# Performance work log

Measured on AMD Instinct MI355X. Metric: run time of the kernel, lower is better.

The kernel has to match this reference:

```python
import jax, jax.numpy as jnp
import numpy as np

B, M, IN_DIM = 8, 2048, 512
N_HEAD, ATTN_DIM = 8, 64
HEAD_DIM = N_HEAD * ATTN_DIM  # 512
SCALE = HEAD_DIM ** (-0.5)


def setup_inputs() -> dict:
    key = jax.random.key(0)
    ks = jax.random.split(key, 5)
    s = IN_DIM ** -0.5
    return {
        "x": jax.random.normal(ks[0], (B, M, IN_DIM), dtype=jnp.float32),
        "Wq": jax.random.normal(ks[1], (IN_DIM, HEAD_DIM), dtype=jnp.float32) * s,
        "Wk": jax.random.normal(ks[2], (IN_DIM, HEAD_DIM), dtype=jnp.float32) * s,
        "Wv": jax.random.normal(ks[3], (IN_DIM, HEAD_DIM), dtype=jnp.float32) * s,
        "Wo": jax.random.normal(ks[4], (HEAD_DIM, IN_DIM), dtype=jnp.float32) * s,
        "bo": jnp.zeros((IN_DIM,), dtype=jnp.float32),
    }


def _split_heads(t):
    # [B, M, H*D] -> [B, H, M, D]
    b, m, _ = t.shape
    return t.reshape(b, m, N_HEAD, ATTN_DIM).transpose(0, 2, 1, 3)


def reference(x, Wq, Wk, Wv, Wo, bo):
    q = _split_heads(x @ Wq)  # bhmd
    k = _split_heads(x @ Wk)
    v = _split_heads(x @ Wv)
    # Faithful to source: logits DIVIDED by scale=head_dim**-0.5 (i.e. * sqrt(head_dim))
    logits = jnp.einsum('bhid,bhjd->bhij', q, k) / SCALE
    scores = jax.nn.softmax(logits, axis=-1)
    weighted = jnp.einsum('bhij,bhjd->bhid', scores, v)  # [B,H,M,D]
    merged = weighted.transpose(0, 2, 1, 3).reshape(x.shape[0], x.shape[1], HEAD_DIM)
    return merged @ Wo + bo
```

## Files before the change

### kernel.cpp

```cpp
#include <hip/hip_runtime.h>
#include <hip/hip_bf16.h>
#include <cstdint>

#define DI __device__ __forceinline__

typedef __attribute__((ext_vector_type(8))) short bf16x8;
typedef __attribute__((ext_vector_type(4))) short s16x4;
typedef __attribute__((ext_vector_type(4))) float f32x4;
typedef __attribute__((ext_vector_type(2))) int   i32x2;

static constexpr int BATCH = 8, SEQ = 2048;
static constexpr int ROWS = BATCH * SEQ;
static constexpr float SCALE_Q = (float)(22.627416997969522 * 1.4426950408889634);

DI short f2bf(float f) { __hip_bfloat16 h = __float2bfloat16(f); return *reinterpret_cast<short*>(&h); }
DI float bf2f(short s) { __hip_bfloat16 h; *reinterpret_cast<short*>(&h) = s; return __bfloat162float(h); }
DI unsigned pack2(float a, float b) {
  return (unsigned)(unsigned short)f2bf(a) | ((unsigned)(unsigned short)f2bf(b) << 16);
}

DI void gload_lds16(const void* gp, void* lp) {
  __builtin_amdgcn_global_load_lds(
      (__attribute__((address_space(1))) void*)const_cast<void*>(gp),
      (__attribute__((address_space(3))) void*)lp, 16, 0, 0);
}
DI f32x4 mfma16(bf16x8 a, bf16x8 b, f32x4 c) {
  return __builtin_amdgcn_mfma_f32_16x16x32_bf16(a, b, c, 0, 0, 0);
}

__global__ __launch_bounds__(256)
void prep_x(const float* __restrict__ x, short* __restrict__ xh, short* __restrict__ xl)
{
  const int g0 = blockIdx.x * 1024 + threadIdx.x;
#pragma unroll
  for (int i = 0; i < 4; ++i) {
    int g = g0 + i * 256;
    const float4 v = *reinterpret_cast<const float4*>(x + (size_t)g * 4);
    s16x4 h4, l4;
#pragma unroll
    for (int j = 0; j < 4; ++j) {
      float f = ((const float*)&v)[j];
      short hb = f2bf(f);
      h4[j] = hb;
      l4[j] = f2bf(f - bf2f(hb));
    }
    *reinterpret_cast<s16x4*>(xh + (size_t)g * 4) = h4;
    *reinterpret_cast<s16x4*>(xl + (size_t)g * 4) = l4;
  }
}

__global__ __launch_bounds__(256)
void prep_w(const float* __restrict__ Wq, const float* __restrict__ Wk,
            const float* __restrict__ Wv, const float* __restrict__ Wo,
            short* __restrict__ Wqk_hi, short* __restrict__ Wqk_lo,
            short* __restrict__ Wv_t, short* __restrict__ Wo_t)
{
  __shared__ float t[64][65];
  const int blk = blockIdx.x;
  const int mat = blk >> 6;
  const int tile = blk & 63;
  const int tn = (tile & 7) * 64;
  const int tk = (tile >> 3) * 64;
  const float* src = mat == 0 ? Wq : mat == 1 ? Wk : mat == 2 ? Wv : Wo;
  const float scale = (mat == 0) ? SCALE_Q : 1.0f;
  const int tid = threadIdx.x;
#pragma unroll
  for (int i = 0; i < 16; ++i) {
    int idx = i * 256 + tid;
    t[idx >> 6][idx & 63] = src[(size_t)(tk + (idx >> 6)) * 512 + tn + (idx & 63)];
  }
  __syncthreads();
#pragma unroll
  for (int i = 0; i < 16; ++i) {
    int idx = i * 256 + tid;
    int nn = idx >> 6, kk = idx & 63;
    float v = t[kk][nn] * scale;
    short hb = f2bf(v);
    size_t o = (size_t)(tn + nn) * 512 + (tk + kk);
    if (mat <= 1) {
      Wqk_hi[(size_t)mat * 512 * 512 + o] = hb;
      Wqk_lo[(size_t)mat * 512 * 512 + o] = f2bf(v - bf2f(hb));
    } else if (mat == 2) Wv_t[o] = hb;
    else Wo_t[o] = hb;
  }
}

template<int MODE>
__global__ __launch_bounds__(256, 2)
void gemm_kern(const short* __restrict__ Axh, const short* __restrict__ Axl,
               const short* __restrict__ Bhg, const short* __restrict__ Blg,
               short* __restrict__ O0h, short* __restrict__ O0l,
               short* __restrict__ O1h, short* __restrict__ O1l,
               float* __restrict__ Of, const float* __restrict__ bias)
{
  constexpr bool SPLIT = (MODE == 0);
  __shared__ __align__(16) short Ah[128 * 32];
  __shared__ __align__(16) short Bh[128 * 32];
  __shared__ __align__(16) short Al[SPLIT ? 128 * 32 : 16];
  __shared__ __align__(16) short Bl[SPLIT ? 128 * 32 : 16];

  const int tid = threadIdx.x;
  const int wave = tid >> 6, lane = tid & 63, lo = lane & 15, hi4 = lane >> 4;
  const int wr = wave >> 1, wc = wave & 1;
  const int m0 = blockIdx.y * 128, n0 = blockIdx.x * 128;

  f32x4 acc[4][4] = {};

  for (int kt = 0; kt < 16; ++kt) {
    __syncthreads();
#pragma unroll
    for (int is = 0; is < 2; ++is) {
      int rowl = is * 64 + wave * 16 + (lane >> 2);
      int chunk = (lane & 3) ^ ((rowl >> 1) & 3);
      size_t ab = ((size_t)(m0 + rowl) * 512 + kt * 32) * 2 + chunk * 16;
      gload_lds16((const char*)Axh + ab, (char*)Ah + is * 4096 + wave * 1024);
      if constexpr (SPLIT)
        gload_lds16((const char*)Axl + ab, (char*)Al + is * 4096 + wave * 1024);
      size_t gb = ((size_t)(n0 + rowl) * 512 + kt * 32) * 2 + chunk * 16;
      gload_lds16((const char*)Bhg + gb, (char*)Bh + is * 4096 + wave * 1024);
      if constexpr (SPLIT)
        gload_lds16((const char*)Blg + gb, (char*)Bl + is * 4096 + wave * 1024);
    }
    __syncthreads();
    bf16x8 a_h[4], a_l[4], b_h[4], b_l[4];
#pragma unroll
    for (int m = 0; m < 4; ++m) {
      int ar = wr * 64 + m * 16 + lo;
      int off = ar * 64 + ((hi4 ^ ((ar >> 1) & 3)) << 4);
      a_h[m] = *reinterpret_cast<const bf16x8*>((const char*)Ah + off);
      if constexpr (SPLIT) a_l[m] = *reinterpret_cast<const bf16x8*>((const char*)Al + off);
    }
#pragma unroll
    for (int n = 0; n < 4; ++n) {
      int br = wc * 64 + n * 16 + lo;
      int off = br * 64 + ((hi4 ^ ((br >> 1) & 3)) << 4);
      b_h[n] = *reinterpret_cast<const bf16x8*>((const char*)Bh + off);
      if constexpr (SPLIT) b_l[n] = *reinterpret_cast<const bf16x8*>((const char*)Bl + off);
    }
    __builtin_amdgcn_s_setprio(1);
#pragma unroll
    for (int m = 0; m < 4; ++m)
#pragma unroll
      for (int n = 0; n < 4; ++n) {
        acc[m][n] = mfma16(a_h[m], b_h[n], acc[m][n]);
        if constexpr (SPLIT) {
          acc[m][n] = mfma16(a_h[m], b_l[n], acc[m][n]);
          acc[m][n] = mfma16(a_l[m], b_h[n], acc[m][n]);
        }
      }
    __builtin_amdgcn_s_setprio(0);
  }
#pragma unroll
  for (int m = 0; m < 4; ++m)
#pragma unroll
    for (int n = 0; n < 4; ++n) {
      if constexpr (MODE == 1) {
        int cg = n0 + wc * 64 + n * 16 + lo;
        int rgb = m0 + wr * 64 + m * 16 + hi4 * 4;
        int bh = (rgb >> 11) * 8 + (cg >> 6);
        s16x4 vt4;
#pragma unroll
        for (int j = 0; j < 4; ++j) vt4[j] = f2bf(acc[m][n][j]);
        size_t o = ((size_t)(bh * 64 + (cg & 63))) * 2048 + (rgb & 2047);
        *reinterpret_cast<s16x4*>(O0h + o) = vt4;
      } else {
#pragma unroll
        for (int j = 0; j < 4; ++j) {
          int rg = m0 + wr * 64 + m * 16 + hi4 * 4 + j;
          int cg = n0 + wc * 64 + n * 16 + lo;
          float v = acc[m][n][j];
          if constexpr (MODE == 2) {
            Of[(size_t)rg * 512 + cg] = v + bias[cg];
          } else {
            int mat = cg >> 9;
            int c9 = cg & 511;
            size_t o = ((size_t)((rg >> 11) * 8 + (c9 >> 6)) * 2048 + (rg & 2047)) * 64 + (c9 & 63);
            short hb = f2bf(v);
            short lb = f2bf(v - bf2f(hb));
            if (mat == 0) { O0h[o] = hb; O0l[o] = lb; }
            else          { O1h[o] = hb; O1l[o] = lb; }
          }
        }
      }
    }
}

__global__ __launch_bounds__(256, 2)
void attn_kern(const short* __restrict__ Qh, const short* __restrict__ Ql,
               const short* __restrict__ Kh, const short* __restrict__ Kl,
               const short* __restrict__ VTg, short* __restrict__ Og)
{
  __shared__ __align__(16) short Ksh[2][64 * 64];
  __shared__ __align__(16) short Ksl[2][64 * 64];
  __shared__ __align__(16) short Vts[2][64 * 64];
  __shared__ __align__(16) short Ps[4][1024];

  const int bh = blockIdx.y, qt = blockIdx.x;
  const int tid = threadIdx.x, wave = tid >> 6, lane = tid & 63, lo = lane & 15, hi4 = lane >> 4;
  const int q0 = qt * 64;

  const size_t qoff = ((size_t)bh * 2048 + q0 + wave * 16 + lo) * 64;
  bf16x8 qh[2], ql[2];
#pragma unroll
  for (int kk = 0; kk < 2; ++kk) {
    qh[kk] = *reinterpret_cast<const bf16x8*>(Qh + qoff + kk * 32 + hi4 * 8);
    ql[kk] = *reinterpret_cast<const bf16x8*>(Ql + qoff + kk * 32 + hi4 * 8);
  }

  f32x4 acc_o[4] = {};
  float m_run = -3.0e38f, l_run = 0.f;

  short* pw = &Ps[wave][0];

  auto STAGE = [&](int kt, int buf) {
#pragma unroll
    for (int is = 0; is < 2; ++is) {
      int rowl = is * 32 + wave * 8 + (lane >> 3);
      int chunk = (lane & 7) ^ (rowl & 7);
      size_t gbK = ((size_t)bh * 2048 + kt * 64 + rowl) * 128 + chunk * 16;
      gload_lds16((const char*)Kh + gbK, (char*)&Ksh[buf][0] + is * 4096 + wave * 1024);
      gload_lds16((const char*)Kl + gbK, (char*)&Ksl[buf][0] + is * 4096 + wave * 1024);
      size_t gbV = (((size_t)bh * 64 + rowl) * 2048 + kt * 64) * 2 + chunk * 16;
      gload_lds16((const char*)VTg + gbV, (char*)&Vts[buf][0] + is * 4096 + wave * 1024);
    }
  };

  STAGE(0, 0);
  __syncthreads();

  for (int kt = 0; kt < 32; ++kt) {
    const int cur = kt & 1;
    if (kt < 31) STAGE(kt + 1, cur ^ 1);

    f32x4 s[4];
    __builtin_amdgcn_s_setprio(1);
#pragma unroll
    for (int kb = 0; kb < 4; ++kb) {
      f32x4 t = {0.f, 0.f, 0.f, 0.f};
#pragma unroll
      for (int kk = 0; kk < 2; ++kk) {
        int krow = kb * 16 + lo;
        int off = krow * 128 + ((kk * 64 + hi4 * 16) ^ ((krow & 7) << 4));
        bf16x8 kh8 = *reinterpret_cast<const bf16x8*>((const char*)&Ksh[cur][0] + off);
        bf16x8 kl8 = *reinterpret_cast<const bf16x8*>((const char*)&Ksl[cur][0] + off);
        t = mfma16(kh8, qh[kk], t);
        t = mfma16(kl8, qh[kk], t);
        t = mfma16(kh8, ql[kk], t);
      }
      s[kb] = t;
    }
    __builtin_amdgcn_s_setprio(0);

    float mt = s[0][0];
#pragma unroll
    for (int kb = 0; kb < 4; ++kb)
#pragma unroll
      for (int j = 0; j < 4; ++j) mt = fmaxf(mt, s[kb][j]);
    mt = fmaxf(mt, __shfl_xor(mt, 16));
    mt = fmaxf(mt, __shfl_xor(mt, 32));
    if (!__all(mt - m_run <= 8.0f)) {
      float mn = fmaxf(m_run, mt);
      float corr = exp2f(m_run - mn);
      m_run = mn;
      l_run *= corr;
#pragma unroll
      for (int j = 0; j < 4; ++j) {
        float cj = __shfl(corr, hi4 * 4 + j);
#pragma unroll
        for (int db = 0; db < 4; ++db) acc_o[db][j] *= cj;
      }
    }
    float ls = 0.f;
#pragma unroll
    for (int kb = 0; kb < 4; ++kb)
#pragma unroll
      for (int j = 0; j < 4; ++j) {
        float p = exp2f(s[kb][j] - m_run);
        s[kb][j] = p;
        ls += p;
      }
    ls += __shfl_xor(ls, 16);
    ls += __shfl_xor(ls, 32);
    l_run += ls;

#pragma unroll
    for (int kb = 0; kb < 4; ++kb) {
      i32x2 w;
      w.x = (int)pack2(s[kb][0], s[kb][1]);
      w.y = (int)pack2(s[kb][2], s[kb][3]);
      int off = lo * 128 + ((kb * 32 + hi4 * 8) ^ ((lo & 7) << 4));
      *reinterpret_cast<i32x2*>((char*)pw + off) = w;
    }
    __builtin_amdgcn_sched_barrier(0);
    bf16x8 pa[2];
#pragma unroll
    for (int kk = 0; kk < 2; ++kk) {
      int off = lo * 128 + ((kk * 64 + hi4 * 16) ^ ((lo & 7) << 4));
      pa[kk] = *reinterpret_cast<const bf16x8*>((const char*)pw + off);
    }

    __builtin_amdgcn_s_setprio(1);
#pragma unroll
    for (int db = 0; db < 4; ++db) {
#pragma unroll
      for (int kk = 0; kk < 2; ++kk) {
        int vrow = db * 16 + lo;
        int voff = vrow * 128 + ((kk * 64 + hi4 * 16) ^ ((lo & 7) << 4));
        bf16x8 v8 = *reinterpret_cast<const bf16x8*>((const char*)&Vts[cur][0] + voff);
        acc_o[db] = mfma16(pa[kk], v8, acc_o[db]);
      }
    }
    __builtin_amdgcn_s_setprio(0);

    __syncthreads();
  }

  const int b = bh >> 3, h = bh & 7;
#pragma unroll
  for (int j = 0; j < 4; ++j) {
    float lr = __shfl(l_run, hi4 * 4 + j);
    float inv = 1.0f / lr;
    int mrow = q0 + wave * 16 + hi4 * 4 + j;
    size_t base = ((size_t)(b * 2048 + mrow)) * 512 + h * 64;
#pragma unroll
    for (int db = 0; db < 4; ++db)
      Og[base + db * 16 + lo] = f2bf(acc_o[db][j] * inv);
  }
}

extern "C" void kernel_launch(void* const* d_in, const int* in_sizes, int n_in,
                              void* d_out, int out_size, void* d_ws, size_t ws_size,
                              hipStream_t stream) {
  const float* x  = (const float*)d_in[0];
  const float* Wq = (const float*)d_in[1];
  const float* Wk = (const float*)d_in[2];
  const float* Wv = (const float*)d_in[3];
  const float* Wo = (const float*)d_in[4];
  const float* bo = (const float*)d_in[5];
  float* out = (float*)d_out;

  char* ws = (char*)d_ws;
  short* Wqk_hi = (short*)(ws);
  short* Wqk_lo = (short*)(ws + (1 << 20));
  short* Wv_t   = (short*)(ws + (2 << 20));
  short* Wo_t   = (short*)(ws + (2 << 20) + 512 * 512 * 2);
  char* big = ws + 3 * (1 << 20);
  const size_t SZ = (size_t)ROWS * 512 * 2;
  short* Qh = (short*)(big);
  short* Ql = (short*)(big + SZ);
  short* Kh = (short*)(big + 2 * SZ);
  short* Kl = (short*)(big + 3 * SZ);
  short* VT = (short*)(big + 4 * SZ);
  short* Ob = (short*)(big + 5 * SZ);
  short* xh = Ob;
  short* xl = (short*)(big + 6 * SZ);
  (void)in_sizes; (void)n_in; (void)out_size; (void)ws_size;

  prep_w<<<dim3(256), dim3(256), 0, stream>>>(Wq, Wk, Wv, Wo, Wqk_hi, Wqk_lo, Wv_t, Wo_t);
  prep_x<<<dim3(2048), dim3(256), 0, stream>>>(x, xh, xl);
  gemm_kern<0><<<dim3(8, 128), dim3(256), 0, stream>>>(xh, xl, Wqk_hi, Wqk_lo,
                                                       Qh, Ql, Kh, Kl, nullptr, nullptr);
  gemm_kern<1><<<dim3(4, 128), dim3(256), 0, stream>>>(xh, nullptr, Wv_t, nullptr,
                                                       VT, nullptr, nullptr, nullptr, nullptr, nullptr);
  attn_kern<<<dim3(32, 64), dim3(256), 0, stream>>>(Qh, Ql, Kh, Kl, VT, Ob);
  gemm_kern<2><<<dim3(4, 128), dim3(256), 0, stream>>>(Ob, nullptr, Wo_t, nullptr,
                                                       nullptr, nullptr, nullptr, nullptr, out, bo);
}
```

Baseline: 429.1 us.

## Process two query row groups per wave and drop K/V double buffering

Each wave now handles 32 query rows as two 16-row groups, so every K/V tile loaded into LDS is reused across twice as many MFMAs, and the grid shrinks to 16 query tiles per head. The K/V LDS double buffer is removed in favour of a single buffer with two barriers per iteration, and the launch bound rises to 4 blocks per CU to rely on occupancy for latency hiding. The aim is to halve K/V global and LDS traffic per query. The cost is more registers per thread, which may conflict with the higher occupancy target, and the loss of explicit prefetch overlap.

```diff
diff --git a/kernel.cpp b/kernel.cpp
--- a/kernel.cpp
+++ b/kernel.cpp
@@ -185,119 +185,127 @@
     }
 }
 
-__global__ __launch_bounds__(256, 2)
+__global__ __launch_bounds__(256, 4)
 void attn_kern(const short* __restrict__ Qh, const short* __restrict__ Ql,
                const short* __restrict__ Kh, const short* __restrict__ Kl,
                const short* __restrict__ VTg, short* __restrict__ Og)
 {
-  __shared__ __align__(16) short Ksh[2][64 * 64];
-  __shared__ __align__(16) short Ksl[2][64 * 64];
-  __shared__ __align__(16) short Vts[2][64 * 64];
-  __shared__ __align__(16) short Ps[4][1024];
+  __shared__ __align__(16) short Ksh[64 * 64];
+  __shared__ __align__(16) short Ksl[64 * 64];
+  __shared__ __align__(16) short Vts[64 * 64];
+  __shared__ __align__(16) short Ps[4][2][1024];
 
   const int bh = blockIdx.y, qt = blockIdx.x;
   const int tid = threadIdx.x, wave = tid >> 6, lane = tid & 63, lo = lane & 15, hi4 = lane >> 4;
-  const int q0 = qt * 64;
-
-  const size_t qoff = ((size_t)bh * 2048 + q0 + wave * 16 + lo) * 64;
-  bf16x8 qh[2], ql[2];
-#pragma unroll
-  for (int kk = 0; kk < 2; ++kk) {
-    qh[kk] = *reinterpret_cast<const bf16x8*>(Qh + qoff + kk * 32 + hi4 * 8);
-    ql[kk] = *reinterpret_cast<const bf16x8*>(Ql + qoff + kk * 32 + hi4 * 8);
-  }
-
-  f32x4 acc_o[4] = {};
-  float m_run = -3.0e38f, l_run = 0.f;
-
-  short* pw = &Ps[wave][0];
-
-  auto STAGE = [&](int kt, int buf) {
+  const int q0 = qt * 128;
+
+  bf16x8 qh[2][2], ql[2][2];
+#pragma unroll
+  for (int g = 0; g < 2; ++g) {
+    const size_t qoff = ((size_t)bh * 2048 + q0 + wave * 32 + g * 16 + lo) * 64;
+#pragma unroll
+    for (int kk = 0; kk < 2; ++kk) {
+      qh[g][kk] = *reinterpret_cast<const bf16x8*>(Qh + qoff + kk * 32 + hi4 * 8);
+      ql[g][kk] = *reinterpret_cast<const bf16x8*>(Ql + qoff + kk * 32 + hi4 * 8);
+    }
+  }
+
+  f32x4 acc_o[2][4] = {};
+  float m_run[2] = {-3.0e38f, -3.0e38f}, l_run[2] = {0.f, 0.f};
+
+  for (int kt = 0; kt < 32; ++kt) {
+    __syncthreads();
 #pragma unroll
     for (int is = 0; is < 2; ++is) {
       int rowl = is * 32 + wave * 8 + (lane >> 3);
       int chunk = (lane & 7) ^ (rowl & 7);
       size_t gbK = ((size_t)bh * 2048 + kt * 64 + rowl) * 128 + chunk * 16;
-      gload_lds16((const char*)Kh + gbK, (char*)&Ksh[buf][0] + is * 4096 + wave * 1024);
-      gload_lds16((const char*)Kl + gbK, (char*)&Ksl[buf][0] + is * 4096 + wave * 1024);
+      gload_lds16((const char*)Kh + gbK, (char*)Ksh + is * 4096 + wave * 1024);
+      gload_lds16((const char*)Kl + gbK, (char*)Ksl + is * 4096 + wave * 1024);
       size_t gbV = (((size_t)bh * 64 + rowl) * 2048 + kt * 64) * 2 + chunk * 16;
-      gload_lds16((const char*)VTg + gbV, (char*)&Vts[buf][0] + is * 4096 + wave * 1024);
-    }
-  };
-
-  STAGE(0, 0);
-  __syncthreads();
-
-  for (int kt = 0; kt < 32; ++kt) {
-    const int cur = kt & 1;
-    if (kt < 31) STAGE(kt + 1, cur ^ 1);
-
-    f32x4 s[4];
+      gload_lds16((const char*)VTg + gbV, (char*)Vts + is * 4096 + wave * 1024);
+    }
+    __syncthreads();
+
+    f32x4 s[2][4];
     __builtin_amdgcn_s_setprio(1);
 #pragma unroll
     for (int kb = 0; kb < 4; ++kb) {
-      f32x4 t = {0.f, 0.f, 0.f, 0.f};
+      f32x4 t0 = {0.f, 0.f, 0.f, 0.f}, t1 = {0.f, 0.f, 0.f, 0.f};
 #pragma unroll
       for (int kk = 0; kk < 2; ++kk) {
         int krow = kb * 16 + lo;
         int off = krow * 128 + ((kk * 64 + hi4 * 16) ^ ((krow & 7) << 4));
-        bf16x8 kh8 = *reinterpret_cast<const bf16x8*>((const char*)&Ksh[cur][0] + off);
-        bf16x8 kl8 = *reinterpret_cast<const bf16x8*>((const char*)&Ksl[cur][0] + off);
-        t = mfma16(kh8, qh[kk], t);
-        t = mfma16(kl8, qh[kk], t);
-        t = mfma16(kh8, ql[kk], t);
-      }
-      s[kb] = t;
+        bf16x8 kh8 = *reinterpret_cast<const bf16x8*>((const char*)Ksh + off);
+        bf16x8 kl8 = *reinterpret_cast<const bf16x8*>((const char*)Ksl + off);
+        t0 = mfma16(kh8, qh[0][kk], t0);
+        t1 = mfma16(kh8, qh[1][kk], t1);
+        t0 = mfma16(kl8, qh[0][kk], t0);
+        t1 = mfma16(kl8, qh[1][kk], t1);
+        t0 = mfma16(kh8, ql[0][kk], t0);
+        t1 = mfma16(kh8, ql[1][kk], t1);
+      }
+      s[0][kb] = t0;
+      s[1][kb] = t1;
     }
     __builtin_amdgcn_s_setprio(0);
 
-    float mt = s[0][0];
-#pragma unroll
-    for (int kb = 0; kb < 4; ++kb)
-#pragma unroll
-      for (int j = 0; j < 4; ++j) mt = fmaxf(mt, s[kb][j]);
-    mt = fmaxf(mt, __shfl_xor(mt, 16));
-    mt = fmaxf(mt, __shfl_xor(mt, 32));
-    if (!__all(mt - m_run <= 8.0f)) {
-      float mn = fmaxf(m_run, mt);
-      float corr = exp2f(m_run - mn);
-      m_run = mn;
-      l_run *= corr;
-#pragma unroll
-      for (int j = 0; j < 4; ++j) {
-        float cj = __shfl(corr, hi4 * 4 + j);
-#pragma unroll
-        for (int db = 0; db < 4; ++db) acc_o[db][j] *= cj;
-      }
-    }
-    float ls = 0.f;
-#pragma unroll
-    for (int kb = 0; kb < 4; ++kb)
-#pragma unroll
-      for (int j = 0; j < 4; ++j) {
-        float p = exp2f(s[kb][j] - m_run);
-        s[kb][j] = p;
-        ls += p;
-      }
-    ls += __shfl_xor(ls, 16);
-    ls += __shfl_xor(ls, 32);
-    l_run += ls;
-
-#pragma unroll
-    for (int kb = 0; kb < 4; ++kb) {
-      i32x2 w;
-      w.x = (int)pack2(s[kb][0], s[kb][1]);
-      w.y = (int)pack2(s[kb][2], s[kb][3]);
-      int off = lo * 128 + ((kb * 32 + hi4 * 8) ^ ((lo & 7) << 4));
-      *reinterpret_cast<i32x2*>((char*)pw + off) = w;
+#pragma unroll
+    for (int g = 0; g < 2; ++g) {
+      float mt = s[g][0][0];
+#pragma unroll
+      for (int kb = 0; kb < 4; ++kb)
+#pragma unroll
+        for (int j = 0; j < 4; ++j) mt = fmaxf(mt, s[g][kb][j]);
+      mt = fmaxf(mt, __shfl_xor(mt, 16));
+      mt = fmaxf(mt, __shfl_xor(mt, 32));
+      if (!__all(mt - m_run[g] <= 8.0f)) {
+        float mn = fmaxf(m_run[g], mt);
+        float corr = exp2f(m_run[g] - mn);
+        m_run[g] = mn;
+        l_run[g] *= corr;
+#pragma unroll
+        for (int j = 0; j < 4; ++j) {
+          float cj = __shfl(corr, hi4 * 4 + j);
+#pragma unroll
+          for (int db = 0; db < 4; ++db) acc_o[g][db][j] *= cj;
+        }
+      }
+      float ls = 0.f;
+#pragma unroll
+      for (int kb = 0; kb < 4; ++kb)
+#pragma unroll
+        for (int j = 0; j < 4; ++j) {
+          float p = exp2f(s[g][kb][j] - m_run[g]);
+          s[g][kb][j] = p;
+          ls += p;
+        }
+      ls += __shfl_xor(ls, 16);
+      ls += __shfl_xor(ls, 32);
+      l_run[g] += ls;
+    }
+
+#pragma unroll
+    for (int g = 0; g < 2; ++g) {
+      char* pw = (char*)&Ps[wave][g][0];
+#pragma unroll
+      for (int kb = 0; kb < 4; ++kb) {
+        i32x2 w;
+        w.x = (int)pack2(s[g][kb][0], s[g][kb][1]);
+        w.y = (int)pack2(s[g][kb][2], s[g][kb][3]);
+        int off = lo * 128 + ((kb * 32 + hi4 * 8) ^ ((lo & 7) << 4));
+        *reinterpret_cast<i32x2*>(pw + off) = w;
+      }
     }
     __builtin_amdgcn_sched_barrier(0);
-    bf16x8 pa[2];
-#pragma unroll
-    for (int kk = 0; kk < 2; ++kk) {
-      int off = lo * 128 + ((kk * 64 + hi4 * 16) ^ ((lo & 7) << 4));
-      pa[kk] = *reinterpret_cast<const bf16x8*>((const char*)pw + off);
-    }
+    bf16x8 pa[2][2];
+#pragma unroll
+    for (int g = 0; g < 2; ++g)
+#pragma unroll
+      for (int kk = 0; kk < 2; ++kk) {
+        int off = lo * 128 + ((kk * 64 + hi4 * 16) ^ ((lo & 7) << 4));
+        pa[g][kk] = *reinterpret_cast<const bf16x8*>((const char*)&Ps[wave][g][0] + off);
+      }
 
     __builtin_amdgcn_s_setprio(1);
 #pragma unroll
@@ -306,26 +314,27 @@
       for (int kk = 0; kk < 2; ++kk) {
         int vrow = db * 16 + lo;
         int voff = vrow * 128 + ((kk * 64 + hi4 * 16) ^ ((lo & 7) << 4));
-        bf16x8 v8 = *reinterpret_cast<const bf16x8*>((const char*)&Vts[cur][0] + voff);
-        acc_o[db] = mfma16(pa[kk], v8, acc_o[db]);
+        bf16x8 v8 = *reinterpret_cast<const bf16x8*>((const char*)Vts + voff);
+        acc_o[0][db] = mfma16(pa[0][kk], v8, acc_o[0][db]);
+        acc_o[1][db] = mfma16(pa[1][kk], v8, acc_o[1][db]);
       }
     }
     __builtin_amdgcn_s_setprio(0);
-
-    __syncthreads();
   }
 
   const int b = bh >> 3, h = bh & 7;
 #pragma unroll
-  for (int j = 0; j < 4; ++j) {
-    float lr = __shfl(l_run, hi4 * 4 + j);
-    float inv = 1.0f / lr;
-    int mrow = q0 + wave * 16 + hi4 * 4 + j;
-    size_t base = ((size_t)(b * 2048 + mrow)) * 512 + h * 64;
-#pragma unroll
-    for (int db = 0; db < 4; ++db)
-      Og[base + db * 16 + lo] = f2bf(acc_o[db][j] * inv);
-  }
+  for (int g = 0; g < 2; ++g)
+#pragma unroll
+    for (int j = 0; j < 4; ++j) {
+      float lr = __shfl(l_run[g], hi4 * 4 + j);
+      float inv = 1.0f / lr;
+      int mrow = q0 + wave * 32 + g * 16 + hi4 * 4 + j;
+      size_t base = ((size_t)(b * 2048 + mrow)) * 512 + h * 64;
+#pragma unroll
+      for (int db = 0; db < 4; ++db)
+        Og[base + db * 16 + lo] = f2bf(acc_o[g][db][j] * inv);
+    }
 }
 
 extern "C" void kernel_launch(void* const* d_in, const int* in_sizes, int n_in,
@@ -362,7 +371,7 @@
                                                        Qh, Ql, Kh, Kl, nullptr, nullptr);
   gemm_kern<1><<<dim3(4, 128), dim3(256), 0, stream>>>(xh, nullptr, Wv_t, nullptr,
                                                        VT, nullptr, nullptr, nullptr, nullptr, nullptr);
-  attn_kern<<<dim3(32, 64), dim3(256), 0, stream>>>(Qh, Ql, Kh, Kl, VT, Ob);
+  attn_kern<<<dim3(16, 64), dim3(256), 0, stream>>>(Qh, Ql, Kh, Kl, VT, Ob);
   gemm_kern<2><<<dim3(4, 128), dim3(256), 0, stream>>>(Ob, nullptr, Wo_t, nullptr,
                                                        nullptr, nullptr, nullptr, nullptr, out, bo);
 }
```

Measured after the change: 402.2 us. -6.3%, faster.
